# Kernel optimization log

Measured on AMD Instinct MI355X. Metric: run time of the kernel, lower is better.

Reference implementation:

```python
import jax, jax.numpy as jnp
import numpy as np
from jax import lax

N, S = 4096, 128
V, E, H = 36, 128, 256

def setup_inputs() -> dict:
    key = jax.random.key(0)
    ks = jax.random.split(key, 12)
    s_e = 1.0  # torch nn.Embedding init ~ N(0,1)
    k_l0 = 1.0 / np.sqrt(H)
    inp = {
        'x': jax.random.randint(ks[0], (N, S), 0, V),
        'emb': jax.random.normal(ks[1], (V, E), jnp.float32) * s_e,
        'W_ih0': jax.random.uniform(ks[2], (4 * H, E), jnp.float32, -k_l0, k_l0),
        'W_hh0': jax.random.uniform(ks[3], (4 * H, H), jnp.float32, -k_l0, k_l0),
        'b_ih0': jax.random.uniform(ks[4], (4 * H,), jnp.float32, -k_l0, k_l0),
        'b_hh0': jax.random.uniform(ks[5], (4 * H,), jnp.float32, -k_l0, k_l0),
        'W_ih1': jax.random.uniform(ks[6], (4 * H, H), jnp.float32, -k_l0, k_l0),
        'W_hh1': jax.random.uniform(ks[7], (4 * H, H), jnp.float32, -k_l0, k_l0),
        'b_ih1': jax.random.uniform(ks[8], (4 * H,), jnp.float32, -k_l0, k_l0),
        'b_hh1': jax.random.uniform(ks[9], (4 * H,), jnp.float32, -k_l0, k_l0),
        'fc_W': jax.random.uniform(ks[10], (V, H), jnp.float32, -k_l0, k_l0),
        'fc_b': jax.random.uniform(ks[11], (V,), jnp.float32, -k_l0, k_l0),
    }
    return inp

def _lstm_layer(seq, W_ih, W_hh, b_ih, b_hh):
    # seq: (N, T, D) -> hidden outputs (N, T, H); PyTorch gate order i,f,g,o
    n = seq.shape[0]
    h_dim = W_hh.shape[1]
    b = b_ih + b_hh
    # precompute input projections for all timesteps (one big GEMM)
    x_proj = jnp.einsum('ntd,gd->ntg', seq, W_ih) + b  # (N, T, 4H)

    def step(carry, xp_t):
        h, c = carry
        gates = xp_t + h @ W_hh.T
        i, f, g, o = jnp.split(gates, 4, axis=-1)
        i = jax.nn.sigmoid(i)
        f = jax.nn.sigmoid(f)
        g = jnp.tanh(g)
        o = jax.nn.sigmoid(o)
        c = f * c + i * g
        h = o * jnp.tanh(c)
        return (h, c), h

    h0 = jnp.zeros((n, h_dim), seq.dtype)
    _, hs = lax.scan(step, (h0, h0), jnp.swapaxes(x_proj, 0, 1))
    return jnp.swapaxes(hs, 0, 1)

def reference(x, emb, W_ih0, W_hh0, b_ih0, b_hh0, W_ih1, W_hh1, b_ih1, b_hh1, fc_W, fc_b):
    # SMILES length: number of non-padding (non-ignore_index=0) tokens
    lengths = jnp.sum(x != 0, axis=1).astype(jnp.float32)  # (N,)
    e = emb[x]                       # (N, S, E)
    inputs = e[:, :-1, :]            # teacher-forced inputs, (N, S-1, E)
    targets = x[:, 1:]               # next tokens, (N, S-1)
    # 2-layer LSTM (eval mode: inter-layer dropout inactive)
    h = _lstm_layer(inputs, W_ih0, W_hh0, b_ih0, b_hh0)
    h = _lstm_layer(h, W_ih1, W_hh1, b_ih1, b_hh1)
    logits = jax.nn.relu(jnp.einsum('nth,vh->ntv', h, fc_W) + fc_b)  # (N, S-1, V)
    log_probs = jax.nn.log_softmax(logits, axis=-1)
    probs = jnp.exp(log_probs)
    nll = -jnp.take_along_axis(log_probs, targets[..., None], axis=-1)[..., 0]
    token_loss = jnp.where(targets == 0, 0.0, nll) / lengths[:, None]
    molecule_loss = jnp.sum(token_loss, axis=1)
    loss = jnp.mean(molecule_loss)
    return probs, molecule_loss, loss
```

## Files before the change

### kernel.cpp

```cpp
#include <hip/hip_runtime.h>

typedef float f32x4 __attribute__((ext_vector_type(4)));
typedef short bf16x8 __attribute__((ext_vector_type(8)));

#define SLEN 128
#define TLEN 127
#define VOC 36
#define NPROBS (4096*127*36)
#define MLOSS_OFF NPROBS
#define LOSS_OFF (NPROBS + 4096)

#define WS_W0 0
#define WS_W1 786432
#define WS_FC 1835008
#define WS_B0 1859584
#define WS_B1 1863680
#define NW0 393216
#define NW1 524288
#define NFC 12288

#define WS_H0  2097152
#define WS_H1  6291456
#define WS_CTR 10485760
#define WS_NEEDED 10518528

#define GRP 131072
#define SLOT 65536

__device__ __forceinline__ short f2bf(float f){
  unsigned u = __float_as_uint(f);
  u += 0x7fffu + ((u >> 16) & 1u);
  return (short)(u >> 16);
}
__device__ __forceinline__ float fsig(float x){ return 1.0f/(1.0f + __expf(-x)); }
__device__ __forceinline__ float ftanh(float x){ return 1.0f - 2.0f/(1.0f + __expf(2.0f*x)); }

__device__ __forceinline__ void ld16_sc(bf16x8* d, const short* p){
  asm volatile("global_load_dwordx4 %0, %1, off sc0 sc1" : "=&v"(*d) : "v"(p));
}
__device__ __forceinline__ void st2_sc(short* p, short v){
  asm volatile("global_store_short %0, %1, off sc0 sc1" :: "v"(p), "v"(v));
}
__device__ __forceinline__ void vmdrain_sb(){
  asm volatile("s_waitcnt vmcnt(0)" ::: "memory");
  __builtin_amdgcn_sched_barrier(0);
}
__device__ __forceinline__ unsigned ldflag_sc(const unsigned* p){
  unsigned r;
  asm volatile("global_load_dword %0, %1, off sc0 sc1\n\ts_waitcnt vmcnt(0)"
               : "=&v"(r) : "v"(p) : "memory");
  return r;
}
__device__ __forceinline__ void stflag_sc(unsigned* p, unsigned v){
  asm volatile("global_store_dword %0, %1, off sc0 sc1" :: "v"(p), "v"(v) : "memory");
}

__global__ void prep_kernel(const float* __restrict__ Wih0, const float* __restrict__ Whh0,
                            const float* __restrict__ bih0, const float* __restrict__ bhh0,
                            const float* __restrict__ Wih1, const float* __restrict__ Whh1,
                            const float* __restrict__ bih1, const float* __restrict__ bhh1,
                            const float* __restrict__ fcW,
                            short* __restrict__ w0, short* __restrict__ w1, short* __restrict__ fcw,
                            float* __restrict__ b0, float* __restrict__ b1,
                            float* __restrict__ out)
{
  int idx = blockIdx.x*256 + threadIdx.x;
  if (idx == 0) out[LOSS_OFF] = 0.0f;
  if (idx < NW0) {
    int wv = idx / 24576;
    int r1 = idx - wv*24576;
    int G  = r1 / 6144;
    int r2 = r1 - G*6144;
    int kt = r2 / 512;
    int r3 = r2 - kt*512;
    int ln = r3 >> 3, e = r3 & 7;
    int row = G*256 + wv*16 + (ln & 15);
    int col = kt*32 + (ln>>4)*8 + e;
    float v = (col < 128) ? Wih0[row*128 + col] : Whh0[row*256 + (col-128)];
    w0[idx] = f2bf(v);
  } else if (idx < NW0 + NW1) {
    int i2 = idx - NW0;
    int wv = i2 / 32768;
    int r1 = i2 - wv*32768;
    int G  = r1 / 8192;
    int r2 = r1 - G*8192;
    int kt = r2 / 512;
    int r3 = r2 - kt*512;
    int ln = r3 >> 3, e = r3 & 7;
    int row = G*256 + wv*16 + (ln & 15);
    int col = kt*32 + (ln>>4)*8 + e;
    float v = (col < 256) ? Wih1[row*256 + col] : Whh1[row*256 + (col-256)];
    w1[i2] = f2bf(v);
  } else if (idx < NW0 + NW1 + NFC) {
    int i2 = idx - (NW0 + NW1);
    int n  = i2 / 4096;
    int r1 = i2 - n*4096;
    int kt = r1 / 512;
    int r3 = r1 - kt*512;
    int ln = r3 >> 3, e = r3 & 7;
    int row = n*16 + (ln & 15);
    int col = kt*32 + (ln>>4)*8 + e;
    fcw[i2] = (row < VOC) ? f2bf(fcW[row*256 + col]) : (short)0;
  } else if (idx < NW0 + NW1 + NFC + 1024) {
    int i2 = idx - (NW0 + NW1 + NFC);
    b0[i2] = bih0[i2] + bhh0[i2];
  } else if (idx < NW0 + NW1 + NFC + 2048) {
    int i2 = idx - (NW0 + NW1 + NFC + 1024);
    b1[i2] = bih1[i2] + bhh1[i2];
  }
}

__global__ __launch_bounds__(1024, 4)
void lstm_fuse(const int* __restrict__ x, const float* __restrict__ emb,
               const float* __restrict__ fcb,
               const short* __restrict__ W0, const short* __restrict__ W1,
               const short* __restrict__ FCW,
               const float* __restrict__ b0, const float* __restrict__ b1,
               short* __restrict__ h0b, short* __restrict__ h1b,
               unsigned* __restrict__ flags,
               float* __restrict__ out)
{
  extern __shared__ short lds[];
  short* Wl0  = lds;
  short* Wl1  = lds + 24576;
  short* fcs  = lds + 57344;
  short* embs = lds + 69632;
  float* invlen_l = (float*)(lds + 74528);

  const int tid  = threadIdx.x;
  const int lane = tid & 63;
  const int w    = tid >> 6;
  const int l15  = lane & 15;
  const int l4   = lane >> 4;

  const int b = blockIdx.x;
  const int g = (b & 7) + 8*(b >> 7);
  const int q = (b >> 3) & 15;

  unsigned* grp_flags = flags + g*512;
  unsigned* my_flag   = grp_flags + q*32;
  short* gh0 = h0b + g*GRP;
  short* gh1 = h1b + g*GRP;

  for (int i = tid; i < 24576; i += 1024) Wl0[i] = W0[q*24576 + i];
  for (int i = tid; i < 32768; i += 1024) Wl1[i] = W1[q*32768 + i];
  for (int i = tid; i < 12288; i += 1024) fcs[i] = FCW[i];
  for (int i = tid; i < 36*128; i += 1024) {
    int r = i >> 7, c = i & 127;
    embs[r*136 + c] = f2bf(emb[i]);
  }
  if (tid < 16) {
    int row = g*256 + q*16 + tid;
    int cnt = 0;
    for (int s = 0; s < SLEN; s++) cnt += (x[(size_t)row*SLEN + s] != 0) ? 1 : 0;
    invlen_l[tid] = 1.0f / (float)cnt;
  }
  __syncthreads();
  if (tid == 0) stflag_sc(my_flag, 1u);

  const int ch = 16*q + l15;
  const float bi0 = b0[ch], bf0 = b0[256+ch], bg0 = b0[512+ch], bo0 = b0[768+ch];
  const float bi1 = b1[ch], bf1 = b1[256+ch], bg1 = b1[512+ch], bo1 = b1[768+ch];
  const bool  v2  = (l15 < 4);
  const float lb0 = fcb[l15], lb1 = fcb[16 + l15];
  const float lb2 = v2 ? fcb[32 + l15] : 0.f;

  float c0s[2][4] = {};
  float c1s[2][4] = {};
  float mloss[4] = {0.f,0.f,0.f,0.f};

  for (int t = 0; t <= 128; t++) {
    int tok0 = 0, tok1 = 0, tg4[4] = {0,0,0,0};
    if (w < 8 && t <= 126) {
      tok0 = x[(size_t)(g*256 + 32*w      + l15)*SLEN + t];
      tok1 = x[(size_t)(g*256 + 32*w + 16 + l15)*SLEN + t];
    }
    if (w == 7 && t >= 2) {
      #pragma unroll
      for (int j = 0; j < 4; j++)
        tg4[j] = x[(size_t)(g*256 + 16*q + 4*l4 + j)*SLEN + (t-1)];
    }

    if (tid < 16) {
      const unsigned* fp = grp_flags + tid*32;
      while (ldflag_sc(fp) < (unsigned)(t+1))
        __builtin_amdgcn_s_sleep(1);
    }
    __syncthreads();

    if (w < 8) {
      if (t <= 126) {
        const short* hsrc = gh0 + ((t^1)&1)*SLOT;
        const short* aA = hsrc + (32*w      + l15)*32 + l4*8;
        const short* aB = hsrc + (32*w + 16 + l15)*32 + l4*8;
        f32x4 acc[2][4] = {};
        #pragma unroll
        for (int kt = 0; kt < 4; kt++) {
          bf16x8 Bf[4];
          #pragma unroll
          for (int G = 0; G < 4; G++)
            Bf[G] = *(const bf16x8*)(Wl0 + (G*12 + kt)*512 + lane*8);
          bf16x8 A0 = *(const bf16x8*)(embs + tok0*136 + kt*32 + l4*8);
          bf16x8 A1 = *(const bf16x8*)(embs + tok1*136 + kt*32 + l4*8);
          #pragma unroll
          for (int G = 0; G < 4; G++) {
            acc[0][G] = __builtin_amdgcn_mfma_f32_16x16x32_bf16(A0, Bf[G], acc[0][G], 0, 0, 0);
            acc[1][G] = __builtin_amdgcn_mfma_f32_16x16x32_bf16(A1, Bf[G], acc[1][G], 0, 0, 0);
          }
        }
        #pragma unroll
        for (int hf = 0; hf < 2; hf++) {
          bf16x8 SA[4], SB[4];
          #pragma unroll
          for (int i = 0; i < 4; i++) {
            ld16_sc(&SA[i], aA + (hf*4 + i)*8192);
            ld16_sc(&SB[i], aB + (hf*4 + i)*8192);
          }
          vmdrain_sb();
          #pragma unroll
          for (int i = 0; i < 4; i++) {
            int kt = 4 + hf*4 + i;
            bf16x8 Bf[4];
            #pragma unroll
            for (int G = 0; G < 4; G++)
              Bf[G] = *(const bf16x8*)(Wl0 + (G*12 + kt)*512 + lane*8);
            #pragma unroll
            for (int G = 0; G < 4; G++) {
              acc[0][G] = __builtin_amdgcn_mfma_f32_16x16x32_bf16(SA[i], Bf[G], acc[0][G], 0, 0, 0);
              acc[1][G] = __builtin_amdgcn_mfma_f32_16x16x32_bf16(SB[i], Bf[G], acc[1][G], 0, 0, 0);
            }
          }
        }
        short* hdst = gh0 + (t&1)*SLOT + (q>>1)*8192 + (q&1)*16 + l15;
        #pragma unroll
        for (int m = 0; m < 2; m++)
          #pragma unroll
          for (int j = 0; j < 4; j++) {
            float iv = fsig (acc[m][0][j] + bi0);
            float fv = fsig (acc[m][1][j] + bf0);
            float gv = ftanh(acc[m][2][j] + bg0);
            float ov = fsig (acc[m][3][j] + bo0);
            float c  = fv * c0s[m][j] + iv * gv;
            c0s[m][j] = c;
            st2_sc(hdst + (32*w + 16*m + 4*l4 + j)*32, f2bf(ov * ftanh(c)));
          }
      }
      if (w == 7 && t >= 2) {
        const short* h1c = gh1 + (t&1)*SLOT;
        const short* fb  = h1c + (16*q + l15)*32 + l4*8;
        f32x4 a3[3] = {};
        #pragma unroll
        for (int hf = 0; hf < 2; hf++) {
          bf16x8 SA[4];
          #pragma unroll
          for (int i = 0; i < 4; i++)
            ld16_sc(&SA[i], fb + (hf*4 + i)*8192);
          vmdrain_sb();
          #pragma unroll
          for (int i = 0; i < 4; i++) {
            int kt = hf*4 + i;
            #pragma unroll
            for (int n = 0; n < 3; n++) {
              bf16x8 Bf = *(const bf16x8*)(fcs + (n*8 + kt)*512 + lane*8);
              a3[n] = __builtin_amdgcn_mfma_f32_16x16x32_bf16(SA[i], Bf, a3[n], 0, 0, 0);
            }
          }
        }
        #pragma unroll
        for (int j = 0; j < 4; j++) {
          float g0 = fmaxf(a3[0][j] + lb0, 0.f);
          float g1 = fmaxf(a3[1][j] + lb1, 0.f);
          float g2 = v2 ? fmaxf(a3[2][j] + lb2, 0.f) : -INFINITY;
          float mx = fmaxf(fmaxf(g0, g1), g2);
          #pragma unroll
          for (int k = 1; k < 16; k <<= 1) mx = fmaxf(mx, __shfl_xor(mx, k, 64));
          float e0 = __expf(g0 - mx), e1 = __expf(g1 - mx);
          float e2 = v2 ? __expf(g2 - mx) : 0.f;
          float sm = e0 + e1 + e2;
          #pragma unroll
          for (int k = 1; k < 16; k <<= 1) sm += __shfl_xor(sm, k, 64);
          float inv = 1.0f / sm;
          int grow = g*256 + 16*q + 4*l4 + j;
          float* po = out + ((size_t)grow*TLEN + (t-2))*VOC;
          __builtin_nontemporal_store(e0 * inv, po + l15);
          __builtin_nontemporal_store(e1 * inv, po + 16 + l15);
          if (v2) __builtin_nontemporal_store(e2 * inv, po + 32 + l15);
          int tg = tg4[j];
          float sel = (tg < 16) ? g0 : ((tg < 32) ? g1 : g2);
          float ltg = __shfl(sel, (lane & 48) | (tg & 15), 64);
          float nll = mx + __logf(sm) - ltg;
          mloss[j] += (tg != 0) ? nll * invlen_l[4*l4 + j] : 0.f;
        }
      }
    } else {
      if (t >= 1 && t <= 127) {
        const int w8 = w - 8;
        const int s  = t - 1;
        const short* h0src = gh0 + (s&1)*SLOT;
        const short* h1src = gh1 + ((s^1)&1)*SLOT;
        const short* s0A = h0src + (32*w8      + l15)*32 + l4*8;
        const short* s0B = h0src + (32*w8 + 16 + l15)*32 + l4*8;
        const short* s1A = h1src + (32*w8      + l15)*32 + l4*8;
        const short* s1B = h1src + (32*w8 + 16 + l15)*32 + l4*8;
        f32x4 acc[2][4] = {};
        #pragma unroll
        for (int hf = 0; hf < 4; hf++) {
          bf16x8 SA[4], SB[4];
          #pragma unroll
          for (int i = 0; i < 4; i++) {
            int kt = hf*4 + i;
            const short* pA = (kt < 8) ? (s0A + kt*8192) : (s1A + (kt-8)*8192);
            const short* pB = (kt < 8) ? (s0B + kt*8192) : (s1B + (kt-8)*8192);
            ld16_sc(&SA[i], pA);
            ld16_sc(&SB[i], pB);
          }
          vmdrain_sb();
          #pragma unroll
          for (int i = 0; i < 4; i++) {
            int kt = hf*4 + i;
            bf16x8 Bf[4];
            #pragma unroll
            for (int G = 0; G < 4; G++)
              Bf[G] = *(const bf16x8*)(Wl1 + (G*16 + kt)*512 + lane*8);
            #pragma unroll
            for (int G = 0; G < 4; G++) {
              acc[0][G] = __builtin_amdgcn_mfma_f32_16x16x32_bf16(SA[i], Bf[G], acc[0][G], 0, 0, 0);
              acc[1][G] = __builtin_amdgcn_mfma_f32_16x16x32_bf16(SB[i], Bf[G], acc[1][G], 0, 0, 0);
            }
          }
        }
        short* hdst = gh1 + (s&1)*SLOT + (q>>1)*8192 + (q&1)*16 + l15;
        #pragma unroll
        for (int m = 0; m < 2; m++)
          #pragma unroll
          for (int j = 0; j < 4; j++) {
            float iv = fsig (acc[m][0][j] + bi1);
            float fv = fsig (acc[m][1][j] + bf1);
            float gv = ftanh(acc[m][2][j] + bg1);
            float ov = fsig (acc[m][3][j] + bo1);
            float c  = fv * c1s[m][j] + iv * gv;
            c1s[m][j] = c;
            st2_sc(hdst + (32*w8 + 16*m + 4*l4 + j)*32, f2bf(ov * ftanh(c)));
          }
      }
    }

    asm volatile("s_waitcnt vmcnt(0)" ::: "memory");
    __syncthreads();
    if (tid == 0 && t < 128)
      stflag_sc(my_flag, (unsigned)(t+2));
  }

  if (w == 7 && l15 == 0) {
    float tot = 0.f;
    #pragma unroll
    for (int j = 0; j < 4; j++) {
      int grow = g*256 + 16*q + 4*l4 + j;
      __builtin_nontemporal_store(mloss[j], out + (size_t)MLOSS_OFF + grow);
      tot += mloss[j];
    }
    atomicAdd(out + LOSS_OFF, tot * (1.0f/4096.0f));
  }
}

__global__ __launch_bounds__(1024, 4)
void lstm_small(const int* __restrict__ x, const float* __restrict__ emb,
                const float* __restrict__ fcb,
                const short* __restrict__ W0, const short* __restrict__ W1,
                const short* __restrict__ FCW,
                const float* __restrict__ b0, const float* __restrict__ b1,
                float* __restrict__ out)
{
  __shared__ __align__(16) short emb_s[36*136];
  __shared__ __align__(16) short h0_s[32*264];
  __shared__ __align__(16) short h1_s[32*264];
  __shared__ int   tok_s[32];
  __shared__ float invlen_s[32];

  const int tid  = threadIdx.x;
  const int lane = tid & 63;
  const int wv   = tid >> 6;
  const int l15  = lane & 15;
  const int l4   = lane >> 4;
  const int r0   = blockIdx.x * 32;

  for (int i = tid; i < 36*128; i += 1024) {
    int r = i >> 7, c = i & 127;
    emb_s[r*136 + c] = f2bf(emb[i]);
  }
  for (int i = tid; i < 32*264; i += 1024) { h0_s[i] = 0; h1_s[i] = 0; }
  if (tid < 32) {
    int cnt = 0;
    for (int s = 0; s < SLEN; s++) cnt += (x[(r0+tid)*SLEN + s] != 0) ? 1 : 0;
    invlen_s[tid] = 1.0f / (float)cnt;
    tok_s[tid] = x[(r0+tid)*SLEN + 0];
  }
  __syncthreads();

  const int ch = wv*16 + l15;
  const short* w0base = W0 + wv*24576 + lane*8;
  const short* w1base = W1 + wv*32768 + lane*8;
  const short* fcbase = FCW + lane*8;
  const float bi0 = b0[ch], bf0 = b0[256+ch], bg0 = b0[512+ch], bo0 = b0[768+ch];
  const float bi1 = b1[ch], bf1 = b1[256+ch], bg1 = b1[512+ch], bo1 = b1[768+ch];
  const bool  v2  = (l15 < 4);
  const float lb0 = fcb[l15], lb1 = fcb[16 + l15];
  const float lb2 = v2 ? fcb[32 + l15] : 0.f;

  float c0s[2][4] = {};
  float c1s[2][4] = {};
  float mloss[4] = {0.f,0.f,0.f,0.f};

  for (int t = 0; t < TLEN; t++) {
    int tokv[2];
    #pragma unroll
    for (int m = 0; m < 2; m++) tokv[m] = tok_s[m*16 + l15];
    float hn0[2][4];
    {
      f32x4 acc[2][4] = {};
      #pragma unroll
      for (int kt = 0; kt < 12; kt++) {
        bf16x8 Bf[4];
        #pragma unroll
        for (int G = 0; G < 4; G++) Bf[G] = *(const bf16x8*)(w0base + (G*12 + kt)*512);
        bf16x8 Af[2];
        #pragma unroll
        for (int m = 0; m < 2; m++) {
          if (kt < 4) Af[m] = *(const bf16x8*)(emb_s + tokv[m]*136 + kt*32 + l4*8);
          else        Af[m] = *(const bf16x8*)(h0_s + (m*16 + l15)*264 + (kt-4)*32 + l4*8);
        }
        #pragma unroll
        for (int m = 0; m < 2; m++)
          #pragma unroll
          for (int G = 0; G < 4; G++)
            acc[m][G] = __builtin_amdgcn_mfma_f32_16x16x32_bf16(Af[m], Bf[G], acc[m][G], 0, 0, 0);
      }
      #pragma unroll
      for (int m = 0; m < 2; m++)
        #pragma unroll
        for (int j = 0; j < 4; j++) {
          float iv = fsig (acc[m][0][j] + bi0);
          float fv = fsig (acc[m][1][j] + bf0);
          float gv = ftanh(acc[m][2][j] + bg0);
          float ov = fsig (acc[m][3][j] + bo0);
          float c  = fv * c0s[m][j] + iv * gv;
          c0s[m][j] = c;
          hn0[m][j] = ov * ftanh(c);
        }
    }
    __syncthreads();
    if (wv == 15 && lane < 32) tok_s[lane] = x[(r0+lane)*SLEN + t + 1];
    #pragma unroll
    for (int m = 0; m < 2; m++)
      #pragma unroll
      for (int j = 0; j < 4; j++)
        h0_s[(m*16 + l4*4 + j)*264 + ch] = f2bf(hn0[m][j]);
    __syncthreads();
    float hn1[2][4];
    {
      f32x4 acc[2][4] = {};
      #pragma unroll
      for (int kt = 0; kt < 16; kt++) {
        bf16x8 Bf[4];
        #pragma unroll
        for (int G = 0; G < 4; G++) Bf[G] = *(const bf16x8*)(w1base + (G*16 + kt)*512);
        bf16x8 Af[2];
        #pragma unroll
        for (int m = 0; m < 2; m++) {
          if (kt < 8) Af[m] = *(const bf16x8*)(h0_s + (m*16 + l15)*264 + kt*32 + l4*8);
          else        Af[m] = *(const bf16x8*)(h1_s + (m*16 + l15)*264 + (kt-8)*32 + l4*8);
        }
        #pragma unroll
        for (int m = 0; m < 2; m++)
          #pragma unroll
          for (int G = 0; G < 4; G++)
            acc[m][G] = __builtin_amdgcn_mfma_f32_16x16x32_bf16(Af[m], Bf[G], acc[m][G], 0, 0, 0);
      }
      #pragma unroll
      for (int m = 0; m < 2; m++)
        #pragma unroll
        for (int j = 0; j < 4; j++) {
          float iv = fsig (acc[m][0][j] + bi1);
          float fv = fsig (acc[m][1][j] + bf1);
          float gv = ftanh(acc[m][2][j] + bg1);
          float ov = fsig (acc[m][3][j] + bo1);
          float c  = fv * c1s[m][j] + iv * gv;
          c1s[m][j] = c;
          hn1[m][j] = ov * ftanh(c);
        }
    }
    __syncthreads();
    #pragma unroll
    for (int m = 0; m < 2; m++)
      #pragma unroll
      for (int j = 0; j < 4; j++)
        h1_s[(m*16 + l4*4 + j)*264 + ch] = f2bf(hn1[m][j]);
    __syncthreads();
    if (wv < 2) {
      const int wr = wv * 16;
      f32x4 a3[3] = {};
      #pragma unroll
      for (int kt = 0; kt < 8; kt++) {
        bf16x8 Ah = *(const bf16x8*)(h1_s + (wr + l15)*264 + kt*32 + l4*8);
        #pragma unroll
        for (int n = 0; n < 3; n++) {
          bf16x8 Bf = *(const bf16x8*)(fcbase + (n*8 + kt)*512);
          a3[n] = __builtin_amdgcn_mfma_f32_16x16x32_bf16(Ah, Bf, a3[n], 0, 0, 0);
        }
      }
      #pragma unroll
      for (int j = 0; j < 4; j++) {
        float g0 = fmaxf(a3[0][j] + lb0, 0.f);
        float g1 = fmaxf(a3[1][j] + lb1, 0.f);
        float g2 = v2 ? fmaxf(a3[2][j] + lb2, 0.f) : -INFINITY;
        float mx = fmaxf(fmaxf(g0, g1), g2);
        #pragma unroll
        for (int k = 1; k < 16; k <<= 1) mx = fmaxf(mx, __shfl_xor(mx, k, 64));
        float e0 = __expf(g0 - mx), e1 = __expf(g1 - mx);
        float e2 = v2 ? __expf(g2 - mx) : 0.f;
        float sm = e0 + e1 + e2;
        #pragma unroll
        for (int k = 1; k < 16; k <<= 1) sm += __shfl_xor(sm, k, 64);
        float inv = 1.0f / sm;
        int row = wr + l4*4 + j;
        float* po = out + ((size_t)(r0 + row)*TLEN + t)*VOC;
        __builtin_nontemporal_store(e0 * inv, po + l15);
        __builtin_nontemporal_store(e1 * inv, po + 16 + l15);
        if (v2) __builtin_nontemporal_store(e2 * inv, po + 32 + l15);
        int tg = tok_s[row];
        float sel = (tg < 16) ? g0 : ((tg < 32) ? g1 : g2);
        float ltg = __shfl(sel, (lane & 48) | (tg & 15), 64);
        float nll = mx + __logf(sm) - ltg;
        mloss[j] += (tg != 0) ? nll * invlen_s[row] : 0.f;
      }
    }
  }
  if (wv < 2 && l15 == 0) {
    float tot = 0.f;
    #pragma unroll
    for (int j = 0; j < 4; j++) {
      int row = wv*16 + l4*4 + j;
      __builtin_nontemporal_store(mloss[j], out + (size_t)MLOSS_OFF + r0 + row);
      tot += mloss[j];
    }
    atomicAdd(out + LOSS_OFF, tot * (1.0f/4096.0f));
  }
}

extern "C" void kernel_launch(void* const* d_in, const int* in_sizes, int n_in,
                              void* d_out, int out_size, void* d_ws, size_t ws_size,
                              hipStream_t stream) {
  const int*   x    = (const int*)  d_in[0];
  const float* emb  = (const float*)d_in[1];
  const float* Wih0 = (const float*)d_in[2];
  const float* Whh0 = (const float*)d_in[3];
  const float* bih0 = (const float*)d_in[4];
  const float* bhh0 = (const float*)d_in[5];
  const float* Wih1 = (const float*)d_in[6];
  const float* Whh1 = (const float*)d_in[7];
  const float* bih1 = (const float*)d_in[8];
  const float* bhh1 = (const float*)d_in[9];
  const float* fcW  = (const float*)d_in[10];
  const float* fcb  = (const float*)d_in[11];

  short* w0  = (short*)((char*)d_ws + WS_W0);
  short* w1  = (short*)((char*)d_ws + WS_W1);
  short* fcw = (short*)((char*)d_ws + WS_FC);
  float* b0  = (float*)((char*)d_ws + WS_B0);
  float* b1  = (float*)((char*)d_ws + WS_B1);
  float* out = (float*)d_out;

  bool big = (ws_size >= (size_t)WS_NEEDED);
  static int lds_ok = -1;
  if (big && lds_ok < 0) {
    hipError_t e = hipFuncSetAttribute((const void*)lstm_fuse,
                     hipFuncAttributeMaxDynamicSharedMemorySize, 149504);
    lds_ok = (e == hipSuccess) ? 1 : 0;
  }
  bool use_pipe = big && (lds_ok == 1);

  short*    h0bp = (short*)((char*)d_ws + WS_H0);
  short*    h1bp = (short*)((char*)d_ws + WS_H1);
  unsigned* ctr  = (unsigned*)((char*)d_ws + WS_CTR);

  prep_kernel<<<3640, 256, 0, stream>>>(Wih0, Whh0, bih0, bhh0, Wih1, Whh1,
                                        bih1, bhh1, fcW, w0, w1, fcw, b0, b1, out);
  if (use_pipe) {
    hipMemsetAsync((char*)d_ws + WS_H0, 0, (size_t)(WS_NEEDED - WS_H0), stream);
    lstm_fuse<<<256, 1024, 149504, stream>>>(x, emb, fcb, w0, w1, fcw, b0, b1,
                                             h0bp, h1bp, ctr, out);
  } else {
    lstm_small<<<128, 1024, 0, stream>>>(x, emb, fcb, w0, w1, fcw, b0, b1, out);
  }
}
```

Baseline: 1.798 ms.

## Give every wave both LSTM layers for 16 rows and share hidden-state loads

Before, waves 0-7 ran layer 0 on 32 rows each and waves 8-15 ran layer 1, with wave 7 alone doing the FC/softmax. Now every wave runs layer 0, layer 1 and its slice of the FC for 16 rows. The h0 fragments loaded once are reused by both layer-0's recurrent GEMM and layer-1's input GEMM, and the FC work is spread across waves (w==q). Loads are issued up front with a partial vmcnt wait so layer-0 and layer-1 MFMAs can overlap with the outstanding h1 loads. The cost is higher register pressure per wave, and each wave now does serial work from both layers, which could lengthen the critical path per step.

```diff
diff --git a/kernel.cpp b/kernel.cpp
--- a/kernel.cpp
+++ b/kernel.cpp
@@ -40,10 +40,6 @@
 }
 __device__ __forceinline__ void st2_sc(short* p, short v){
   asm volatile("global_store_short %0, %1, off sc0 sc1" :: "v"(p), "v"(v));
-}
-__device__ __forceinline__ void vmdrain_sb(){
-  asm volatile("s_waitcnt vmcnt(0)" ::: "memory");
-  __builtin_amdgcn_sched_barrier(0);
 }
 __device__ __forceinline__ unsigned ldflag_sc(const unsigned* p){
   unsigned r;
@@ -165,20 +161,29 @@
   const float lb0 = fcb[l15], lb1 = fcb[16 + l15];
   const float lb2 = v2 ? fcb[32 + l15] : 0.f;
 
-  float c0s[2][4] = {};
-  float c1s[2][4] = {};
+  const int myrow = g*256 + 16*w + l15;
+  const int abase = (16*w + l15)*32 + l4*8;
+  const int sbase = (q>>1)*8192 + (q&1)*16 + l15;
+
+  float c0s[4] = {}, c1s[4] = {};
   float mloss[4] = {0.f,0.f,0.f,0.f};
 
   for (int t = 0; t <= 128; t++) {
-    int tok0 = 0, tok1 = 0, tg4[4] = {0,0,0,0};
-    if (w < 8 && t <= 126) {
-      tok0 = x[(size_t)(g*256 + 32*w      + l15)*SLEN + t];
-      tok1 = x[(size_t)(g*256 + 32*w + 16 + l15)*SLEN + t];
-    }
-    if (w == 7 && t >= 2) {
-      #pragma unroll
-      for (int j = 0; j < 4; j++)
+    const bool doL0 = (t <= 126);
+    const bool doL1 = (t >= 1 && t <= 127);
+    const bool doFC = (w == q) && (t >= 2);
+
+    int tok = 0;
+    if (doL0) tok = x[(size_t)myrow*SLEN + t];
+    int embb = tok*136 + l4*8;
+    asm volatile("" : "+v"(embb));
+    int tg4[4] = {0,0,0,0};
+    if (doFC) {
+      #pragma unroll
+      for (int j = 0; j < 4; j++) {
         tg4[j] = x[(size_t)(g*256 + 16*q + 4*l4 + j)*SLEN + (t-1)];
+        asm volatile("" : "+v"(tg4[j]));
+      }
     }
 
     if (tid < 16) {
@@ -188,160 +193,127 @@
     }
     __syncthreads();
 
-    if (w < 8) {
-      if (t <= 126) {
-        const short* hsrc = gh0 + ((t^1)&1)*SLOT;
-        const short* aA = hsrc + (32*w      + l15)*32 + l4*8;
-        const short* aB = hsrc + (32*w + 16 + l15)*32 + l4*8;
-        f32x4 acc[2][4] = {};
-        #pragma unroll
-        for (int kt = 0; kt < 4; kt++) {
-          bf16x8 Bf[4];
-          #pragma unroll
-          for (int G = 0; G < 4; G++)
-            Bf[G] = *(const bf16x8*)(Wl0 + (G*12 + kt)*512 + lane*8);
-          bf16x8 A0 = *(const bf16x8*)(embs + tok0*136 + kt*32 + l4*8);
-          bf16x8 A1 = *(const bf16x8*)(embs + tok1*136 + kt*32 + l4*8);
-          #pragma unroll
-          for (int G = 0; G < 4; G++) {
-            acc[0][G] = __builtin_amdgcn_mfma_f32_16x16x32_bf16(A0, Bf[G], acc[0][G], 0, 0, 0);
-            acc[1][G] = __builtin_amdgcn_mfma_f32_16x16x32_bf16(A1, Bf[G], acc[1][G], 0, 0, 0);
-          }
-        }
-        #pragma unroll
-        for (int hf = 0; hf < 2; hf++) {
-          bf16x8 SA[4], SB[4];
-          #pragma unroll
-          for (int i = 0; i < 4; i++) {
-            ld16_sc(&SA[i], aA + (hf*4 + i)*8192);
-            ld16_sc(&SB[i], aB + (hf*4 + i)*8192);
-          }
-          vmdrain_sb();
-          #pragma unroll
-          for (int i = 0; i < 4; i++) {
-            int kt = 4 + hf*4 + i;
-            bf16x8 Bf[4];
-            #pragma unroll
-            for (int G = 0; G < 4; G++)
-              Bf[G] = *(const bf16x8*)(Wl0 + (G*12 + kt)*512 + lane*8);
-            #pragma unroll
-            for (int G = 0; G < 4; G++) {
-              acc[0][G] = __builtin_amdgcn_mfma_f32_16x16x32_bf16(SA[i], Bf[G], acc[0][G], 0, 0, 0);
-              acc[1][G] = __builtin_amdgcn_mfma_f32_16x16x32_bf16(SB[i], Bf[G], acc[1][G], 0, 0, 0);
-            }
-          }
-        }
-        short* hdst = gh0 + (t&1)*SLOT + (q>>1)*8192 + (q&1)*16 + l15;
-        #pragma unroll
-        for (int m = 0; m < 2; m++)
-          #pragma unroll
-          for (int j = 0; j < 4; j++) {
-            float iv = fsig (acc[m][0][j] + bi0);
-            float fv = fsig (acc[m][1][j] + bf0);
-            float gv = ftanh(acc[m][2][j] + bg0);
-            float ov = fsig (acc[m][3][j] + bo0);
-            float c  = fv * c0s[m][j] + iv * gv;
-            c0s[m][j] = c;
-            st2_sc(hdst + (32*w + 16*m + 4*l4 + j)*32, f2bf(ov * ftanh(c)));
-          }
-      }
-      if (w == 7 && t >= 2) {
-        const short* h1c = gh1 + (t&1)*SLOT;
-        const short* fb  = h1c + (16*q + l15)*32 + l4*8;
-        f32x4 a3[3] = {};
-        #pragma unroll
-        for (int hf = 0; hf < 2; hf++) {
-          bf16x8 SA[4];
-          #pragma unroll
-          for (int i = 0; i < 4; i++)
-            ld16_sc(&SA[i], fb + (hf*4 + i)*8192);
-          vmdrain_sb();
-          #pragma unroll
-          for (int i = 0; i < 4; i++) {
-            int kt = hf*4 + i;
-            #pragma unroll
-            for (int n = 0; n < 3; n++) {
-              bf16x8 Bf = *(const bf16x8*)(fcs + (n*8 + kt)*512 + lane*8);
-              a3[n] = __builtin_amdgcn_mfma_f32_16x16x32_bf16(SA[i], Bf, a3[n], 0, 0, 0);
-            }
-          }
-        }
-        #pragma unroll
-        for (int j = 0; j < 4; j++) {
-          float g0 = fmaxf(a3[0][j] + lb0, 0.f);
-          float g1 = fmaxf(a3[1][j] + lb1, 0.f);
-          float g2 = v2 ? fmaxf(a3[2][j] + lb2, 0.f) : -INFINITY;
-          float mx = fmaxf(fmaxf(g0, g1), g2);
-          #pragma unroll
-          for (int k = 1; k < 16; k <<= 1) mx = fmaxf(mx, __shfl_xor(mx, k, 64));
-          float e0 = __expf(g0 - mx), e1 = __expf(g1 - mx);
-          float e2 = v2 ? __expf(g2 - mx) : 0.f;
-          float sm = e0 + e1 + e2;
-          #pragma unroll
-          for (int k = 1; k < 16; k <<= 1) sm += __shfl_xor(sm, k, 64);
-          float inv = 1.0f / sm;
-          int grow = g*256 + 16*q + 4*l4 + j;
-          float* po = out + ((size_t)grow*TLEN + (t-2))*VOC;
-          __builtin_nontemporal_store(e0 * inv, po + l15);
-          __builtin_nontemporal_store(e1 * inv, po + 16 + l15);
-          if (v2) __builtin_nontemporal_store(e2 * inv, po + 32 + l15);
-          int tg = tg4[j];
-          float sel = (tg < 16) ? g0 : ((tg < 32) ? g1 : g2);
-          float ltg = __shfl(sel, (lane & 48) | (tg & 15), 64);
-          float nll = mx + __logf(sm) - ltg;
-          mloss[j] += (tg != 0) ? nll * invlen_l[4*l4 + j] : 0.f;
-        }
-      }
-    } else {
-      if (t >= 1 && t <= 127) {
-        const int w8 = w - 8;
-        const int s  = t - 1;
-        const short* h0src = gh0 + (s&1)*SLOT;
-        const short* h1src = gh1 + ((s^1)&1)*SLOT;
-        const short* s0A = h0src + (32*w8      + l15)*32 + l4*8;
-        const short* s0B = h0src + (32*w8 + 16 + l15)*32 + l4*8;
-        const short* s1A = h1src + (32*w8      + l15)*32 + l4*8;
-        const short* s1B = h1src + (32*w8 + 16 + l15)*32 + l4*8;
-        f32x4 acc[2][4] = {};
-        #pragma unroll
-        for (int hf = 0; hf < 4; hf++) {
-          bf16x8 SA[4], SB[4];
-          #pragma unroll
-          for (int i = 0; i < 4; i++) {
-            int kt = hf*4 + i;
-            const short* pA = (kt < 8) ? (s0A + kt*8192) : (s1A + (kt-8)*8192);
-            const short* pB = (kt < 8) ? (s0B + kt*8192) : (s1B + (kt-8)*8192);
-            ld16_sc(&SA[i], pA);
-            ld16_sc(&SB[i], pB);
-          }
-          vmdrain_sb();
-          #pragma unroll
-          for (int i = 0; i < 4; i++) {
-            int kt = hf*4 + i;
-            bf16x8 Bf[4];
-            #pragma unroll
-            for (int G = 0; G < 4; G++)
-              Bf[G] = *(const bf16x8*)(Wl1 + (G*16 + kt)*512 + lane*8);
-            #pragma unroll
-            for (int G = 0; G < 4; G++) {
-              acc[0][G] = __builtin_amdgcn_mfma_f32_16x16x32_bf16(SA[i], Bf[G], acc[0][G], 0, 0, 0);
-              acc[1][G] = __builtin_amdgcn_mfma_f32_16x16x32_bf16(SB[i], Bf[G], acc[1][G], 0, 0, 0);
-            }
-          }
-        }
-        short* hdst = gh1 + (s&1)*SLOT + (q>>1)*8192 + (q&1)*16 + l15;
-        #pragma unroll
-        for (int m = 0; m < 2; m++)
-          #pragma unroll
-          for (int j = 0; j < 4; j++) {
-            float iv = fsig (acc[m][0][j] + bi1);
-            float fv = fsig (acc[m][1][j] + bf1);
-            float gv = ftanh(acc[m][2][j] + bg1);
-            float ov = fsig (acc[m][3][j] + bo1);
-            float c  = fv * c1s[m][j] + iv * gv;
-            c1s[m][j] = c;
-            st2_sc(hdst + (32*w8 + 16*m + 4*l4 + j)*32, f2bf(ov * ftanh(c)));
-          }
+    const short* h0src = gh0 + ((t^1)&1)*SLOT + abase;
+    const short* h1src = gh1 + (t&1)*SLOT     + abase;
+    bf16x8 SA[8], SB[8];
+    #pragma unroll
+    for (int i = 0; i < 8; i++) ld16_sc(&SA[i], h0src + i*8192);
+    #pragma unroll
+    for (int i = 0; i < 8; i++) ld16_sc(&SB[i], h1src + i*8192);
+
+    f32x4 acc0[4] = {}, acc1[4] = {};
+
+    if (doL0) {
+      #pragma unroll
+      for (int kt = 0; kt < 4; kt++) {
+        bf16x8 A = *(const bf16x8*)(embs + embb + kt*32);
+        #pragma unroll
+        for (int G = 0; G < 4; G++) {
+          bf16x8 Bf = *(const bf16x8*)(Wl0 + (G*12 + kt)*512 + lane*8);
+          acc0[G] = __builtin_amdgcn_mfma_f32_16x16x32_bf16(A, Bf, acc0[G], 0, 0, 0);
+        }
+      }
+    }
+
+    asm volatile("s_waitcnt vmcnt(8)" ::: "memory");
+    __builtin_amdgcn_sched_barrier(0);
+
+    if (doL0) {
+      #pragma unroll
+      for (int i = 0; i < 8; i++) {
+        #pragma unroll
+        for (int G = 0; G < 4; G++) {
+          bf16x8 Bf = *(const bf16x8*)(Wl0 + (G*12 + 4 + i)*512 + lane*8);
+          acc0[G] = __builtin_amdgcn_mfma_f32_16x16x32_bf16(SA[i], Bf, acc0[G], 0, 0, 0);
+        }
+      }
+    }
+    if (doL1) {
+      #pragma unroll
+      for (int i = 0; i < 8; i++) {
+        #pragma unroll
+        for (int G = 0; G < 4; G++) {
+          bf16x8 Bf = *(const bf16x8*)(Wl1 + (G*16 + i)*512 + lane*8);
+          acc1[G] = __builtin_amdgcn_mfma_f32_16x16x32_bf16(SA[i], Bf, acc1[G], 0, 0, 0);
+        }
+      }
+    }
+
+    asm volatile("s_waitcnt vmcnt(0)" ::: "memory");
+    __builtin_amdgcn_sched_barrier(0);
+
+    if (doL1) {
+      #pragma unroll
+      for (int i = 0; i < 8; i++) {
+        #pragma unroll
+        for (int G = 0; G < 4; G++) {
+          bf16x8 Bf = *(const bf16x8*)(Wl1 + (G*16 + 8 + i)*512 + lane*8);
+          acc1[G] = __builtin_amdgcn_mfma_f32_16x16x32_bf16(SB[i], Bf, acc1[G], 0, 0, 0);
+        }
+      }
+    }
+
+    if (doL0) {
+      short* hdst = gh0 + (t&1)*SLOT + sbase;
+      #pragma unroll
+      for (int j = 0; j < 4; j++) {
+        float iv = fsig (acc0[0][j] + bi0);
+        float fv = fsig (acc0[1][j] + bf0);
+        float gv = ftanh(acc0[2][j] + bg0);
+        float ov = fsig (acc0[3][j] + bo0);
+        float c  = fv * c0s[j] + iv * gv;
+        c0s[j] = c;
+        st2_sc(hdst + (16*w + 4*l4 + j)*32, f2bf(ov * ftanh(c)));
+      }
+    }
+    if (doL1) {
+      short* hdst = gh1 + ((t^1)&1)*SLOT + sbase;
+      #pragma unroll
+      for (int j = 0; j < 4; j++) {
+        float iv = fsig (acc1[0][j] + bi1);
+        float fv = fsig (acc1[1][j] + bf1);
+        float gv = ftanh(acc1[2][j] + bg1);
+        float ov = fsig (acc1[3][j] + bo1);
+        float c  = fv * c1s[j] + iv * gv;
+        c1s[j] = c;
+        st2_sc(hdst + (16*w + 4*l4 + j)*32, f2bf(ov * ftanh(c)));
+      }
+    }
+
+    if (doFC) {
+      f32x4 a3[3] = {};
+      #pragma unroll
+      for (int i = 0; i < 8; i++) {
+        #pragma unroll
+        for (int n = 0; n < 3; n++) {
+          bf16x8 Bf = *(const bf16x8*)(fcs + (n*8 + i)*512 + lane*8);
+          a3[n] = __builtin_amdgcn_mfma_f32_16x16x32_bf16(SB[i], Bf, a3[n], 0, 0, 0);
+        }
+      }
+      #pragma unroll
+      for (int j = 0; j < 4; j++) {
+        float g0 = fmaxf(a3[0][j] + lb0, 0.f);
+        float g1 = fmaxf(a3[1][j] + lb1, 0.f);
+        float g2 = v2 ? fmaxf(a3[2][j] + lb2, 0.f) : -INFINITY;
+        float mx = fmaxf(fmaxf(g0, g1), g2);
+        #pragma unroll
+        for (int k = 1; k < 16; k <<= 1) mx = fmaxf(mx, __shfl_xor(mx, k, 64));
+        float e0 = __expf(g0 - mx), e1 = __expf(g1 - mx);
+        float e2 = v2 ? __expf(g2 - mx) : 0.f;
+        float sm = e0 + e1 + e2;
+        #pragma unroll
+        for (int k = 1; k < 16; k <<= 1) sm += __shfl_xor(sm, k, 64);
+        float inv = 1.0f / sm;
+        int grow = g*256 + 16*q + 4*l4 + j;
+        float* po = out + ((size_t)grow*TLEN + (t-2))*VOC;
+        __builtin_nontemporal_store(e0 * inv, po + l15);
+        __builtin_nontemporal_store(e1 * inv, po + 16 + l15);
+        if (v2) __builtin_nontemporal_store(e2 * inv, po + 32 + l15);
+        int tg = tg4[j];
+        float sel = (tg < 16) ? g0 : ((tg < 32) ? g1 : g2);
+        float ltg = __shfl(sel, (lane & 48) | (tg & 15), 64);
+        float nll = mx + __logf(sm) - ltg;
+        mloss[j] += (tg != 0) ? nll * invlen_l[4*l4 + j] : 0.f;
       }
     }
 
@@ -351,7 +323,7 @@
       stflag_sc(my_flag, (unsigned)(t+2));
   }
 
-  if (w == 7 && l15 == 0) {
+  if (w == q && l15 == 0) {
     float tot = 0.f;
     #pragma unroll
     for (int j = 0; j < 4; j++) {
```

After: 2.219 ms. +23.4%, slower.
